# Kernel optimization log

Hardware: AMD Instinct MI355X
Metric: run time of the kernel (lower is better)

## Reference

```python
import jax, jax.numpy as jnp
import numpy as np

TOP_K = 8


def setup_inputs() -> dict:
    key = jax.random.key(0)
    ks = jax.random.split(key, 5)
    B, S, H, E, I = 2, 1024, 2048, 64, 768
    return {
        "hidden_states": jax.random.normal(ks[0], (B, S, H), dtype=jnp.float32),
        "router_w": jax.random.normal(ks[1], (H, E), dtype=jnp.float32) * 0.02,
        "gate_w": jax.random.normal(ks[2], (E, H, I), dtype=jnp.float32) * 0.02,
        "up_w": jax.random.normal(ks[3], (E, H, I), dtype=jnp.float32) * 0.02,
        "down_w": jax.random.normal(ks[4], (E, I, H), dtype=jnp.float32) * 0.02,
    }


def reference(hidden_states, router_w, gate_w, up_w, down_w):
    B, S, H = hidden_states.shape
    E = router_w.shape[1]
    x = hidden_states.reshape(-1, H)                      # [T, H]
    T = x.shape[0]

    router_logits = x @ router_w                           # [T, E]
    probs = jax.nn.softmax(router_logits.astype(jnp.float32), axis=-1)
    topk_w, topk_idx = jax.lax.top_k(probs, TOP_K)         # [T, K]
    topk_w = topk_w / jnp.sum(topk_w, axis=-1, keepdims=True)  # norm_topk_prob
    topk_w = topk_w.astype(x.dtype)

    # Dense combine weights: zero for non-selected experts -> same math as the
    # gather/scatter loop, jit-friendly (no data-dependent shapes).
    combine = jnp.zeros((T, E), dtype=x.dtype)
    combine = combine.at[jnp.arange(T)[:, None], topk_idx].set(topk_w)  # [T, E]

    g = jnp.einsum('th,ehi->tei', x, gate_w)               # [T, E, I]
    u = jnp.einsum('th,ehi->tei', x, up_w)                 # [T, E, I]
    h = jax.nn.silu(g) * u                                 # SwiGLU
    out = jnp.einsum('te,tei,eih->th', combine, h, down_w)  # weighted combine

    return out.reshape(B, S, H), router_logits
```

## Files before the change

kernel.cpp:

```cpp
#include <hip/hip_runtime.h>
#include <hip/hip_bf16.h>

typedef __hip_bfloat16 bf16;
typedef short s16x8 __attribute__((ext_vector_type(8)));
typedef unsigned short u16x8 __attribute__((ext_vector_type(8)));
typedef float f32x4 __attribute__((ext_vector_type(4)));

#define T_TOK 2048
#define HDIM  2048
#define NEXP  64
#define IDIM  768
#define TOPK  8
#define OUT_OFF (T_TOK * HDIM)
#define NPAIR (T_TOK * TOPK)

#define WS_TOPK_IDX  0
#define WS_TOPK_W    (64 * 1024)
#define WS_PAIR_TOK  (128 * 1024)
#define WS_SLOT_OF   (192 * 1024)
#define WS_COUNTS    (256 * 1024)
#define WS_OFFSETS   (257 * 1024)
#define WS_CURSOR    (258 * 1024)
#define WS_H         (1024 * 1024)
#define WS_PARTIAL   (WS_H + (size_t)NPAIR * IDIM * 2)
#define WS_XB        WS_PARTIAL

__device__ __forceinline__ float bf_to_f(unsigned short u) {
    return __uint_as_float(((unsigned int)u) << 16);
}
__device__ __forceinline__ unsigned short f2bf(float f) {
    unsigned int u = __float_as_uint(f);
    unsigned int r = (u + 0x7FFFu + ((u >> 16) & 1u)) >> 16;
    return (unsigned short)r;
}
__device__ __forceinline__ unsigned cvtpk(float lo, float hi) {
    unsigned r;
    asm("v_cvt_pk_bf16_f32 %0, %1, %2" : "=v"(r) : "v"(lo), "v"(hi));
    return r;
}

typedef const __attribute__((address_space(1))) unsigned int* gas_ptr;
typedef __attribute__((address_space(3))) unsigned int* las_ptr;
__device__ __forceinline__ void gload_lds16(const void* g, void* l) {
    __builtin_amdgcn_global_load_lds((gas_ptr)g, (las_ptr)l, 16, 0, 0);
}

__global__ __launch_bounds__(256) void xbf_kernel(const float* __restrict__ x,
                                                  unsigned short* __restrict__ xb) {
    int i = blockIdx.x * 256 + threadIdx.x;
    const float4* src = (const float4*)x + (size_t)i * 2;
    float4 a = src[0], b = src[1];
    u16x8 o;
    o[0] = f2bf(a.x); o[1] = f2bf(a.y); o[2] = f2bf(a.z); o[3] = f2bf(a.w);
    o[4] = f2bf(b.x); o[5] = f2bf(b.y); o[6] = f2bf(b.z); o[7] = f2bf(b.w);
    ((u16x8*)xb)[i] = o;
}

__global__ __launch_bounds__(256) void router_kernel(
    const float* __restrict__ x, const float* __restrict__ rw,
    float* __restrict__ logits) {
    int wave = threadIdx.x >> 6;
    int lane = threadIdx.x & 63;
    int t = blockIdx.x * 4 + wave;
    const float4* x4 = (const float4*)(x + (size_t)t * HDIM);
    float acc = 0.f;
    for (int h4 = 0; h4 < HDIM / 4; ++h4) {
        float4 xv = x4[h4];
        int h = h4 * 4;
        acc = fmaf(xv.x, rw[(h + 0) * NEXP + lane], acc);
        acc = fmaf(xv.y, rw[(h + 1) * NEXP + lane], acc);
        acc = fmaf(xv.z, rw[(h + 2) * NEXP + lane], acc);
        acc = fmaf(xv.w, rw[(h + 3) * NEXP + lane], acc);
    }
    logits[t * NEXP + lane] = acc;
}

__global__ __launch_bounds__(64) void topk_kernel(
    const float* __restrict__ logits, int* __restrict__ topk_idx,
    float* __restrict__ topk_w, int* __restrict__ counts) {
    int t = blockIdx.x;
    int lane = threadIdx.x;
    float lg = logits[t * NEXP + lane];
    float mx = lg;
    for (int off = 32; off; off >>= 1) mx = fmaxf(mx, __shfl_xor(mx, off));
    float ex = expf(lg - mx);
    float sum = ex;
    for (int off = 32; off; off >>= 1) sum += __shfl_xor(sum, off);
    float prob = ex / sum;

    float pr = prob;
    float myv = 0.f;
    int myidx = 0;
    float ksum = 0.f;
    for (int k = 0; k < TOPK; ++k) {
        float v = pr;
        int idx = lane;
        for (int off = 32; off; off >>= 1) {
            float ov = __shfl_xor(v, off);
            int oi = __shfl_xor(idx, off);
            if (ov > v || (ov == v && oi < idx)) { v = ov; idx = oi; }
        }
        ksum += v;
        if (lane == k) { myidx = idx; myv = v; }
        if (lane == idx) pr = -1.f;
    }
    if (lane < TOPK) {
        topk_idx[t * TOPK + lane] = myidx;
        topk_w[t * TOPK + lane] = myv / ksum;
        atomicAdd(&counts[myidx], 1);
    }
}

__global__ __launch_bounds__(64) void scan_kernel(
    const int* __restrict__ counts, int* __restrict__ offsets, int* __restrict__ cursor) {
    int lane = threadIdx.x;
    int c = counts[lane];
    int incl = c;
    for (int off = 1; off < 64; off <<= 1) {
        int tt = __shfl_up(incl, off);
        if (lane >= off) incl += tt;
    }
    offsets[lane] = incl - c;
    if (lane == 63) offsets[64] = incl;
    cursor[lane] = 0;
}

__global__ __launch_bounds__(256) void scatter_kernel(
    const int* __restrict__ topk_idx, const int* __restrict__ offsets,
    int* __restrict__ cursor, int* __restrict__ pair_token, int* __restrict__ slot_of) {
    int i = blockIdx.x * 256 + threadIdx.x;
    if (i >= NPAIR) return;
    int t = i >> 3;
    int e = topk_idx[i];
    int pos = atomicAdd(&cursor[e], 1);
    int slot = offsets[e] + pos;
    pair_token[slot] = t;
    slot_of[i] = slot;
}

#define BM   128
#define BKS  64

__global__ __launch_bounds__(512, 4) void gateup_mfma(
    const unsigned short* __restrict__ xb, const float* __restrict__ gate_w,
    const float* __restrict__ up_w, const int* __restrict__ offsets,
    const int* __restrict__ pair_token, unsigned short* __restrict__ hbuf) {
    int e = blockIdx.x;
    int ntile = blockIdx.z;
    int off = offsets[e];
    int cnt = offsets[e + 1] - off;
    if (cnt <= 0) return;

    __shared__ unsigned short As[2][BM * BKS];
    __shared__ unsigned short Bgu[2][BM * BKS];
    __shared__ int toks[BM];

    int tid = threadIdx.x;
    int lane = tid & 63;
    int wave = tid >> 6;
    int wr = wave >> 2, wc = wave & 3;
    int l15 = lane & 15, lg4 = lane >> 4;

    int mat = tid >> 8;
    int t8 = tid & 255;
    int nI2 = t8 & 31, kC = t8 >> 5;
    int brow0 = mat * 64 + nI2 * 2;
    int bslot = (kC ^ (nI2 & 7)) * 8;
    const float* bsrc = (mat ? up_w : gate_w) + (size_t)e * HDIM * IDIM
                        + (size_t)(kC * 8) * IDIM + ntile * 64 + nI2 * 2;

    for (int mt = blockIdx.y; mt * BM < cnt; mt += gridDim.y) {
        int m0 = mt * BM;
        if (tid < BM) {
            int p = m0 + tid;
            toks[tid] = pair_token[off + (p < cnt ? p : 0)];
        }
        __syncthreads();
        const unsigned short* aq[2];
        #pragma unroll
        for (int q = 0; q < 2; ++q) {
            int row = q * 64 + (tid >> 3);
            aq[q] = xb + (size_t)toks[row] * HDIM + (((tid & 7) ^ (row & 7)) * 8);
        }
        f32x4 accg[4] = {};
        f32x4 accu[4] = {};

        #pragma unroll
        for (int q = 0; q < 2; ++q)
            gload_lds16(aq[q], &As[0][(q * 512 + tid) * 8]);
        float2 Bv[8];
        #pragma unroll
        for (int i = 0; i < 8; ++i)
            Bv[i] = *(const float2*)(bsrc + (size_t)i * IDIM);

        for (int ks = 0; ks < HDIM / BKS; ++ks) {
            int p = ks & 1;
            {
                uint4 w0, w1;
                w0.x = cvtpk(Bv[0].x, Bv[1].x); w0.y = cvtpk(Bv[2].x, Bv[3].x);
                w0.z = cvtpk(Bv[4].x, Bv[5].x); w0.w = cvtpk(Bv[6].x, Bv[7].x);
                w1.x = cvtpk(Bv[0].y, Bv[1].y); w1.y = cvtpk(Bv[2].y, Bv[3].y);
                w1.z = cvtpk(Bv[4].y, Bv[5].y); w1.w = cvtpk(Bv[6].y, Bv[7].y);
                *(uint4*)&Bgu[p][brow0 * BKS + bslot] = w0;
                *(uint4*)&Bgu[p][(brow0 + 1) * BKS + bslot] = w1;
            }
            __syncthreads();
            if (ks + 1 < HDIM / BKS) {
                int h1 = (ks + 1) * BKS;
                #pragma unroll
                for (int q = 0; q < 2; ++q)
                    gload_lds16(aq[q] + h1, &As[p ^ 1][(q * 512 + tid) * 8]);
                #pragma unroll
                for (int i = 0; i < 8; ++i)
                    Bv[i] = *(const float2*)(bsrc + (size_t)(h1 + i) * IDIM);
            }
            #pragma unroll
            for (int kk = 0; kk < 2; ++kk) {
                int jk = kk * 4 + lg4;
                s16x8 a[4], bg, bu;
                #pragma unroll
                for (int mr = 0; mr < 4; ++mr) {
                    int r = wr * 64 + mr * 16 + l15;
                    a[mr] = *(const s16x8*)&As[p][r * BKS + ((jk ^ (r & 7)) * 8)];
                }
                int rg = wc * 16 + l15;
                int ru = 64 + rg;
                bg = *(const s16x8*)&Bgu[p][rg * BKS + ((jk ^ ((rg >> 1) & 7)) * 8)];
                bu = *(const s16x8*)&Bgu[p][ru * BKS + ((jk ^ ((ru >> 1) & 7)) * 8)];
                #pragma unroll
                for (int mr = 0; mr < 4; ++mr) {
                    accg[mr] = __builtin_amdgcn_mfma_f32_16x16x32_bf16(a[mr], bg, accg[mr], 0, 0, 0);
                    accu[mr] = __builtin_amdgcn_mfma_f32_16x16x32_bf16(a[mr], bu, accu[mr], 0, 0, 0);
                }
            }
        }

        int col = ntile * 64 + wc * 16 + l15;
        #pragma unroll
        for (int mr = 0; mr < 4; ++mr) {
            #pragma unroll
            for (int reg = 0; reg < 4; ++reg) {
                int r = m0 + wr * 64 + mr * 16 + lg4 * 4 + reg;
                if (r < cnt) {
                    float g = accg[mr][reg];
                    float u = accu[mr][reg];
                    float hv = (g / (1.f + __expf(-g))) * u;
                    hbuf[(size_t)(off + r) * IDIM + col] = f2bf(hv);
                }
            }
        }
        __syncthreads();
    }
}

__global__ __launch_bounds__(512, 4) void down_mfma(
    const unsigned short* __restrict__ hbuf, const float* __restrict__ down_w,
    const int* __restrict__ offsets, unsigned short* __restrict__ partial) {
    int e = blockIdx.x;
    int ntile = blockIdx.z;
    int off = offsets[e];
    int cnt = offsets[e + 1] - off;
    if (cnt <= 0) return;

    __shared__ unsigned short As[2][BM * BKS];
    __shared__ unsigned short Bd[2][BM * BKS];

    int tid = threadIdx.x;
    int lane = tid & 63;
    int wave = tid >> 6;
    int wr = wave >> 2, wc = wave & 3;
    int l15 = lane & 15, lg4 = lane >> 4;

    int nI2 = tid & 63, kC = tid >> 6;
    int brow0 = nI2 * 2;
    int bslot = (kC ^ (nI2 & 7)) * 8;
    const float* bsrc = down_w + (size_t)e * IDIM * HDIM
                        + (size_t)(kC * 8) * HDIM + ntile * 128 + nI2 * 2;

    for (int mt = blockIdx.y; mt * BM < cnt; mt += gridDim.y) {
        int m0 = mt * BM;
        const unsigned short* aq[2];
        #pragma unroll
        for (int q = 0; q < 2; ++q) {
            int row = q * 64 + (tid >> 3);
            int rr = m0 + row;
            if (rr >= cnt) rr = cnt - 1;
            aq[q] = hbuf + (size_t)(off + rr) * IDIM + (((tid & 7) ^ (row & 7)) * 8);
        }
        f32x4 acc[4][2] = {};

        #pragma unroll
        for (int q = 0; q < 2; ++q)
            gload_lds16(aq[q], &As[0][(q * 512 + tid) * 8]);
        float2 Bv[8];
        #pragma unroll
        for (int i = 0; i < 8; ++i)
            Bv[i] = *(const float2*)(bsrc + (size_t)i * HDIM);

        for (int ks = 0; ks < IDIM / BKS; ++ks) {
            int p = ks & 1;
            {
                uint4 w0, w1;
                w0.x = cvtpk(Bv[0].x, Bv[1].x); w0.y = cvtpk(Bv[2].x, Bv[3].x);
                w0.z = cvtpk(Bv[4].x, Bv[5].x); w0.w = cvtpk(Bv[6].x, Bv[7].x);
                w1.x = cvtpk(Bv[0].y, Bv[1].y); w1.y = cvtpk(Bv[2].y, Bv[3].y);
                w1.z = cvtpk(Bv[4].y, Bv[5].y); w1.w = cvtpk(Bv[6].y, Bv[7].y);
                *(uint4*)&Bd[p][brow0 * BKS + bslot] = w0;
                *(uint4*)&Bd[p][(brow0 + 1) * BKS + bslot] = w1;
            }
            __syncthreads();
            if (ks + 1 < IDIM / BKS) {
                int k1 = (ks + 1) * BKS;
                #pragma unroll
                for (int q = 0; q < 2; ++q)
                    gload_lds16(aq[q] + k1, &As[p ^ 1][(q * 512 + tid) * 8]);
                #pragma unroll
                for (int i = 0; i < 8; ++i)
                    Bv[i] = *(const float2*)(bsrc + (size_t)(k1 + i) * HDIM);
            }
            #pragma unroll
            for (int kk = 0; kk < 2; ++kk) {
                int jk = kk * 4 + lg4;
                s16x8 a[4], b[2];
                #pragma unroll
                for (int mr = 0; mr < 4; ++mr) {
                    int r = wr * 64 + mr * 16 + l15;
                    a[mr] = *(const s16x8*)&As[p][r * BKS + ((jk ^ (r & 7)) * 8)];
                }
                #pragma unroll
                for (int nr = 0; nr < 2; ++nr) {
                    int row = wc * 32 + nr * 16 + l15;
                    b[nr] = *(const s16x8*)&Bd[p][row * BKS + ((jk ^ ((row >> 1) & 7)) * 8)];
                }
                #pragma unroll
                for (int mr = 0; mr < 4; ++mr)
                    #pragma unroll
                    for (int nr = 0; nr < 2; ++nr)
                        acc[mr][nr] = __builtin_amdgcn_mfma_f32_16x16x32_bf16(
                            a[mr], b[nr], acc[mr][nr], 0, 0, 0);
            }
        }

        #pragma unroll
        for (int mr = 0; mr < 4; ++mr)
            #pragma unroll
            for (int nr = 0; nr < 2; ++nr) {
                int col = ntile * 128 + wc * 32 + nr * 16 + l15;
                #pragma unroll
                for (int reg = 0; reg < 4; ++reg) {
                    int r = m0 + wr * 64 + mr * 16 + lg4 * 4 + reg;
                    if (r < cnt)
                        partial[(size_t)(off + r) * HDIM + col] = f2bf(acc[mr][nr][reg]);
                }
            }
        __syncthreads();
    }
}

__global__ __launch_bounds__(256) void reduce_kernel(
    const unsigned short* __restrict__ partial, const int* __restrict__ slot_of,
    const float* __restrict__ topk_w, float* __restrict__ out) {
    int t = blockIdx.x;
    int j8 = threadIdx.x * 8;
    __shared__ int ss[8];
    __shared__ float sw[8];
    if (threadIdx.x < 8) {
        ss[threadIdx.x] = slot_of[t * TOPK + threadIdx.x];
        sw[threadIdx.x] = topk_w[t * TOPK + threadIdx.x];
    }
    __syncthreads();
    float acc[8] = {};
    #pragma unroll
    for (int k = 0; k < TOPK; ++k) {
        u16x8 v = *(const u16x8*)&partial[(size_t)ss[k] * HDIM + j8];
        float w = sw[k];
        #pragma unroll
        for (int i = 0; i < 8; ++i)
            acc[i] = fmaf(w, bf_to_f((unsigned short)v[i]), acc[i]);
    }
    float4 o0 = {acc[0], acc[1], acc[2], acc[3]};
    float4 o1 = {acc[4], acc[5], acc[6], acc[7]};
    *(float4*)&out[(size_t)t * HDIM + j8] = o0;
    *(float4*)&out[(size_t)t * HDIM + j8 + 4] = o1;
}

extern "C" void kernel_launch(void* const* d_in, const int* in_sizes, int n_in,
                              void* d_out, int out_size, void* d_ws, size_t ws_size,
                              hipStream_t stream) {
    const float* x  = (const float*)d_in[0];
    const float* rw = (const float*)d_in[1];
    const float* gw = (const float*)d_in[2];
    const float* uw = (const float*)d_in[3];
    const float* dw = (const float*)d_in[4];
    float* out = (float*)d_out;
    float* logits = out + OUT_OFF;

    char* ws = (char*)d_ws;
    int*   topk_idx   = (int*)(ws + WS_TOPK_IDX);
    float* topk_w     = (float*)(ws + WS_TOPK_W);
    int*   pair_token = (int*)(ws + WS_PAIR_TOK);
    int*   slot_of    = (int*)(ws + WS_SLOT_OF);
    int*   counts     = (int*)(ws + WS_COUNTS);
    int*   offsets    = (int*)(ws + WS_OFFSETS);
    int*   cursor     = (int*)(ws + WS_CURSOR);
    unsigned short* hbuf    = (unsigned short*)(ws + WS_H);
    unsigned short* partial = (unsigned short*)(ws + WS_PARTIAL);
    unsigned short* xb      = (unsigned short*)(ws + WS_XB);

    hipMemsetAsync(counts, 0, NEXP * sizeof(int), stream);
    xbf_kernel<<<T_TOK * HDIM / (256 * 8), 256, 0, stream>>>(x, xb);
    router_kernel<<<T_TOK / 4, 256, 0, stream>>>(x, rw, logits);
    topk_kernel<<<T_TOK, 64, 0, stream>>>(logits, topk_idx, topk_w, counts);
    scan_kernel<<<1, 64, 0, stream>>>(counts, offsets, cursor);
    scatter_kernel<<<NPAIR / 256, 256, 0, stream>>>(topk_idx, offsets, cursor, pair_token, slot_of);
    gateup_mfma<<<dim3(NEXP, 4, IDIM / 64), 512, 0, stream>>>(xb, gw, uw, offsets, pair_token, hbuf);
    down_mfma<<<dim3(NEXP, 4, HDIM / 128), 512, 0, stream>>>(hbuf, dw, offsets, partial);
    reduce_kernel<<<dim3(T_TOK, 1), 256, 0, stream>>>(partial, slot_of, topk_w, out);
}
```

Measured before the change: 674.1 us.

## Double-buffer weight registers and deepen prefetch with explicit waitcnt scheduling in MoE GEMMs

Both expert GEMM kernels now hold two register sets of fp32 weights, so weight loads are issued two K-steps ahead instead of one. The loop is unrolled by two and uses hand-placed s_waitcnt vmcnt(8) plus raw s_barrier and sched_barrier fences in place of __syncthreads. Each step then waits only for the older LDS-bound activation loads while the newer weight loads stay in flight. This is meant to hide more of the global-memory latency of streaming fp32 weights, at the cost of more VGPRs and fragile ordering assumptions about the memory counter.

```diff
diff --git a/kernel.cpp b/kernel.cpp
--- a/kernel.cpp
+++ b/kernel.cpp
@@ -140,6 +140,62 @@
 
 #define BM   128
 #define BKS  64
+#define NKG  (HDIM / BKS)
+#define NKD  (IDIM / BKS)
+
+#define GU_STEP(KS, BV, P)                                                    \
+  {                                                                           \
+            \
+    uint4 w0, w1;                                                             \
+    w0.x = cvtpk(BV[0].x, BV[1].x); w0.y = cvtpk(BV[2].x, BV[3].x);           \
+    w0.z = cvtpk(BV[4].x, BV[5].x); w0.w = cvtpk(BV[6].x, BV[7].x);           \
+    w1.x = cvtpk(BV[0].y, BV[1].y); w1.y = cvtpk(BV[2].y, BV[3].y);           \
+    w1.z = cvtpk(BV[4].y, BV[5].y); w1.w = cvtpk(BV[6].y, BV[7].y);           \
+    *(uint4*)&Bgu[P][brow0 * BKS + bslot] = w0;                               \
+    *(uint4*)&Bgu[P][(brow0 + 1) * BKS + bslot] = w1;                         \
+    __builtin_amdgcn_sched_barrier(0);                                        \
+    if ((KS) + 1 < NKG) {                                                     \
+      asm volatile("s_waitcnt vmcnt(8) lgkmcnt(0)" ::: "memory");             \
+    } else {                                                                  \
+      asm volatile("s_waitcnt vmcnt(0) lgkmcnt(0)" ::: "memory");             \
+    }                                                                         \
+    __builtin_amdgcn_s_barrier();                                             \
+    __builtin_amdgcn_sched_barrier(0);                                        \
+        \
+    if ((KS) + 1 < NKG) {                                                     \
+      int h1 = ((KS) + 1) * BKS;                                              \
+      gload_lds16(aq[0] + h1, &As[(P) ^ 1][(0 * 512 + tid) * 8]);             \
+      gload_lds16(aq[1] + h1, &As[(P) ^ 1][(1 * 512 + tid) * 8]);             \
+      __builtin_amdgcn_sched_barrier(0);                                      \
+    }                                                                         \
+    if ((KS) + 2 < NKG) {                                                     \
+      int h2 = ((KS) + 2) * BKS;                                              \
+      _Pragma("unroll")                                                       \
+      for (int i = 0; i < 8; ++i)                                             \
+        BV[i] = *(const float2*)(bsrc + (size_t)(h2 + i) * IDIM);             \
+      __builtin_amdgcn_sched_barrier(0);                                      \
+    }                                                                         \
+                                                    \
+    _Pragma("unroll")                                                         \
+    for (int kk = 0; kk < 2; ++kk) {                                          \
+      int jk = kk * 4 + lg4;                                                  \
+      s16x8 a[4], bg, bu;                                                     \
+      _Pragma("unroll")                                                       \
+      for (int mr = 0; mr < 4; ++mr) {                                        \
+        int r = wr * 64 + mr * 16 + l15;                                      \
+        a[mr] = *(const s16x8*)&As[P][r * BKS + ((jk ^ (r & 7)) * 8)];        \
+      }                                                                       \
+      int rg = wc * 16 + l15;                                                 \
+      int ru = 64 + rg;                                                       \
+      bg = *(const s16x8*)&Bgu[P][rg * BKS + ((jk ^ ((rg >> 1) & 7)) * 8)];   \
+      bu = *(const s16x8*)&Bgu[P][ru * BKS + ((jk ^ ((ru >> 1) & 7)) * 8)];   \
+      _Pragma("unroll")                                                       \
+      for (int mr = 0; mr < 4; ++mr) {                                        \
+        accg[mr] = __builtin_amdgcn_mfma_f32_16x16x32_bf16(a[mr], bg, accg[mr], 0, 0, 0); \
+        accu[mr] = __builtin_amdgcn_mfma_f32_16x16x32_bf16(a[mr], bu, accu[mr], 0, 0, 0); \
+      }                                                                       \
+    }                                                                         \
+  }
 
 __global__ __launch_bounds__(512, 4) void gateup_mfma(
     const unsigned short* __restrict__ xb, const float* __restrict__ gate_w,
@@ -157,8 +213,7 @@
 
     int tid = threadIdx.x;
     int lane = tid & 63;
-    int wave = tid >> 6;
-    int wr = wave >> 2, wc = wave & 3;
+    int wr = (tid >> 6) >> 2, wc = (tid >> 6) & 3;
     int l15 = lane & 15, lg4 = lane >> 4;
 
     int mat = tid >> 8;
@@ -185,54 +240,22 @@
         f32x4 accg[4] = {};
         f32x4 accu[4] = {};
 
-        #pragma unroll
-        for (int q = 0; q < 2; ++q)
-            gload_lds16(aq[q], &As[0][(q * 512 + tid) * 8]);
-        float2 Bv[8];
+        gload_lds16(aq[0], &As[0][(0 * 512 + tid) * 8]);
+        gload_lds16(aq[1], &As[0][(1 * 512 + tid) * 8]);
+        __builtin_amdgcn_sched_barrier(0);
+        float2 BvA[8], BvB[8];
         #pragma unroll
         for (int i = 0; i < 8; ++i)
-            Bv[i] = *(const float2*)(bsrc + (size_t)i * IDIM);
-
-        for (int ks = 0; ks < HDIM / BKS; ++ks) {
-            int p = ks & 1;
-            {
-                uint4 w0, w1;
-                w0.x = cvtpk(Bv[0].x, Bv[1].x); w0.y = cvtpk(Bv[2].x, Bv[3].x);
-                w0.z = cvtpk(Bv[4].x, Bv[5].x); w0.w = cvtpk(Bv[6].x, Bv[7].x);
-                w1.x = cvtpk(Bv[0].y, Bv[1].y); w1.y = cvtpk(Bv[2].y, Bv[3].y);
-                w1.z = cvtpk(Bv[4].y, Bv[5].y); w1.w = cvtpk(Bv[6].y, Bv[7].y);
-                *(uint4*)&Bgu[p][brow0 * BKS + bslot] = w0;
-                *(uint4*)&Bgu[p][(brow0 + 1) * BKS + bslot] = w1;
-            }
-            __syncthreads();
-            if (ks + 1 < HDIM / BKS) {
-                int h1 = (ks + 1) * BKS;
-                #pragma unroll
-                for (int q = 0; q < 2; ++q)
-                    gload_lds16(aq[q] + h1, &As[p ^ 1][(q * 512 + tid) * 8]);
-                #pragma unroll
-                for (int i = 0; i < 8; ++i)
-                    Bv[i] = *(const float2*)(bsrc + (size_t)(h1 + i) * IDIM);
-            }
-            #pragma unroll
-            for (int kk = 0; kk < 2; ++kk) {
-                int jk = kk * 4 + lg4;
-                s16x8 a[4], bg, bu;
-                #pragma unroll
-                for (int mr = 0; mr < 4; ++mr) {
-                    int r = wr * 64 + mr * 16 + l15;
-                    a[mr] = *(const s16x8*)&As[p][r * BKS + ((jk ^ (r & 7)) * 8)];
-                }
-                int rg = wc * 16 + l15;
-                int ru = 64 + rg;
-                bg = *(const s16x8*)&Bgu[p][rg * BKS + ((jk ^ ((rg >> 1) & 7)) * 8)];
-                bu = *(const s16x8*)&Bgu[p][ru * BKS + ((jk ^ ((ru >> 1) & 7)) * 8)];
-                #pragma unroll
-                for (int mr = 0; mr < 4; ++mr) {
-                    accg[mr] = __builtin_amdgcn_mfma_f32_16x16x32_bf16(a[mr], bg, accg[mr], 0, 0, 0);
-                    accu[mr] = __builtin_amdgcn_mfma_f32_16x16x32_bf16(a[mr], bu, accu[mr], 0, 0, 0);
-                }
-            }
+            BvA[i] = *(const float2*)(bsrc + (size_t)i * IDIM);
+        __builtin_amdgcn_sched_barrier(0);
+        #pragma unroll
+        for (int i = 0; i < 8; ++i)
+            BvB[i] = *(const float2*)(bsrc + (size_t)(BKS + i) * IDIM);
+        __builtin_amdgcn_sched_barrier(0);
+
+        for (int ks = 0; ks < NKG; ks += 2) {
+            GU_STEP(ks, BvA, 0);
+            GU_STEP(ks + 1, BvB, 1);
         }
 
         int col = ntile * 64 + wc * 16 + l15;
@@ -249,9 +272,60 @@
                 }
             }
         }
-        __syncthreads();
-    }
-}
+    }
+}
+
+#define DN_STEP(KS, BV, P)                                                    \
+  {                                                                           \
+    uint4 w0, w1;                                                             \
+    w0.x = cvtpk(BV[0].x, BV[1].x); w0.y = cvtpk(BV[2].x, BV[3].x);           \
+    w0.z = cvtpk(BV[4].x, BV[5].x); w0.w = cvtpk(BV[6].x, BV[7].x);           \
+    w1.x = cvtpk(BV[0].y, BV[1].y); w1.y = cvtpk(BV[2].y, BV[3].y);           \
+    w1.z = cvtpk(BV[4].y, BV[5].y); w1.w = cvtpk(BV[6].y, BV[7].y);           \
+    *(uint4*)&Bd[P][brow0 * BKS + bslot] = w0;                                \
+    *(uint4*)&Bd[P][(brow0 + 1) * BKS + bslot] = w1;                          \
+    __builtin_amdgcn_sched_barrier(0);                                        \
+    if ((KS) + 1 < NKD) {                                                     \
+      asm volatile("s_waitcnt vmcnt(8) lgkmcnt(0)" ::: "memory");             \
+    } else {                                                                  \
+      asm volatile("s_waitcnt vmcnt(0) lgkmcnt(0)" ::: "memory");             \
+    }                                                                         \
+    __builtin_amdgcn_s_barrier();                                             \
+    __builtin_amdgcn_sched_barrier(0);                                        \
+    if ((KS) + 1 < NKD) {                                                     \
+      int k1 = ((KS) + 1) * BKS;                                              \
+      gload_lds16(aq[0] + k1, &As[(P) ^ 1][(0 * 512 + tid) * 8]);             \
+      gload_lds16(aq[1] + k1, &As[(P) ^ 1][(1 * 512 + tid) * 8]);             \
+      __builtin_amdgcn_sched_barrier(0);                                      \
+    }                                                                         \
+    if ((KS) + 2 < NKD) {                                                     \
+      int k2 = ((KS) + 2) * BKS;                                              \
+      _Pragma("unroll")                                                       \
+      for (int i = 0; i < 8; ++i)                                             \
+        BV[i] = *(const float2*)(bsrc + (size_t)(k2 + i) * HDIM);             \
+      __builtin_amdgcn_sched_barrier(0);                                      \
+    }                                                                         \
+    _Pragma("unroll")                                                         \
+    for (int kk = 0; kk < 2; ++kk) {                                          \
+      int jk = kk * 4 + lg4;                                                  \
+      s16x8 a[4], b[2];                                                       \
+      _Pragma("unroll")                                                       \
+      for (int mr = 0; mr < 4; ++mr) {                                        \
+        int r = wr * 64 + mr * 16 + l15;                                      \
+        a[mr] = *(const s16x8*)&As[P][r * BKS + ((jk ^ (r & 7)) * 8)];        \
+      }                                                                       \
+      _Pragma("unroll")                                                       \
+      for (int nr = 0; nr < 2; ++nr) {                                        \
+        int row = wc * 32 + nr * 16 + l15;                                    \
+        b[nr] = *(const s16x8*)&Bd[P][row * BKS + ((jk ^ ((row >> 1) & 7)) * 8)]; \
+      }                                                                       \
+      _Pragma("unroll")                                                       \
+      for (int mr = 0; mr < 4; ++mr)                                          \
+        _Pragma("unroll")                                                     \
+        for (int nr = 0; nr < 2; ++nr)                                        \
+          acc[mr][nr] = __builtin_amdgcn_mfma_f32_16x16x32_bf16(a[mr], b[nr], acc[mr][nr], 0, 0, 0); \
+    }                                                                         \
+  }
 
 __global__ __launch_bounds__(512, 4) void down_mfma(
     const unsigned short* __restrict__ hbuf, const float* __restrict__ down_w,
@@ -267,8 +341,7 @@
 
     int tid = threadIdx.x;
     int lane = tid & 63;
-    int wave = tid >> 6;
-    int wr = wave >> 2, wc = wave & 3;
+    int wr = (tid >> 6) >> 2, wc = (tid >> 6) & 3;
     int l15 = lane & 15, lg4 = lane >> 4;
 
     int nI2 = tid & 63, kC = tid >> 6;
@@ -279,6 +352,7 @@
 
     for (int mt = blockIdx.y; mt * BM < cnt; mt += gridDim.y) {
         int m0 = mt * BM;
+        __syncthreads();
         const unsigned short* aq[2];
         #pragma unroll
         for (int q = 0; q < 2; ++q) {
@@ -289,56 +363,22 @@
         }
         f32x4 acc[4][2] = {};
 
-        #pragma unroll
-        for (int q = 0; q < 2; ++q)
-            gload_lds16(aq[q], &As[0][(q * 512 + tid) * 8]);
-        float2 Bv[8];
+        gload_lds16(aq[0], &As[0][(0 * 512 + tid) * 8]);
+        gload_lds16(aq[1], &As[0][(1 * 512 + tid) * 8]);
+        __builtin_amdgcn_sched_barrier(0);
+        float2 BvA[8], BvB[8];
         #pragma unroll
         for (int i = 0; i < 8; ++i)
-            Bv[i] = *(const float2*)(bsrc + (size_t)i * HDIM);
-
-        for (int ks = 0; ks < IDIM / BKS; ++ks) {
-            int p = ks & 1;
-            {
-                uint4 w0, w1;
-                w0.x = cvtpk(Bv[0].x, Bv[1].x); w0.y = cvtpk(Bv[2].x, Bv[3].x);
-                w0.z = cvtpk(Bv[4].x, Bv[5].x); w0.w = cvtpk(Bv[6].x, Bv[7].x);
-                w1.x = cvtpk(Bv[0].y, Bv[1].y); w1.y = cvtpk(Bv[2].y, Bv[3].y);
-                w1.z = cvtpk(Bv[4].y, Bv[5].y); w1.w = cvtpk(Bv[6].y, Bv[7].y);
-                *(uint4*)&Bd[p][brow0 * BKS + bslot] = w0;
-                *(uint4*)&Bd[p][(brow0 + 1) * BKS + bslot] = w1;
-            }
-            __syncthreads();
-            if (ks + 1 < IDIM / BKS) {
-                int k1 = (ks + 1) * BKS;
-                #pragma unroll
-                for (int q = 0; q < 2; ++q)
-                    gload_lds16(aq[q] + k1, &As[p ^ 1][(q * 512 + tid) * 8]);
-                #pragma unroll
-                for (int i = 0; i < 8; ++i)
-                    Bv[i] = *(const float2*)(bsrc + (size_t)(k1 + i) * HDIM);
-            }
-            #pragma unroll
-            for (int kk = 0; kk < 2; ++kk) {
-                int jk = kk * 4 + lg4;
-                s16x8 a[4], b[2];
-                #pragma unroll
-                for (int mr = 0; mr < 4; ++mr) {
-                    int r = wr * 64 + mr * 16 + l15;
-                    a[mr] = *(const s16x8*)&As[p][r * BKS + ((jk ^ (r & 7)) * 8)];
-                }
-                #pragma unroll
-                for (int nr = 0; nr < 2; ++nr) {
-                    int row = wc * 32 + nr * 16 + l15;
-                    b[nr] = *(const s16x8*)&Bd[p][row * BKS + ((jk ^ ((row >> 1) & 7)) * 8)];
-                }
-                #pragma unroll
-                for (int mr = 0; mr < 4; ++mr)
-                    #pragma unroll
-                    for (int nr = 0; nr < 2; ++nr)
-                        acc[mr][nr] = __builtin_amdgcn_mfma_f32_16x16x32_bf16(
-                            a[mr], b[nr], acc[mr][nr], 0, 0, 0);
-            }
+            BvA[i] = *(const float2*)(bsrc + (size_t)i * HDIM);
+        __builtin_amdgcn_sched_barrier(0);
+        #pragma unroll
+        for (int i = 0; i < 8; ++i)
+            BvB[i] = *(const float2*)(bsrc + (size_t)(BKS + i) * HDIM);
+        __builtin_amdgcn_sched_barrier(0);
+
+        for (int ks = 0; ks < NKD; ks += 2) {
+            DN_STEP(ks, BvA, 0);
+            DN_STEP(ks + 1, BvB, 1);
         }
 
         #pragma unroll
@@ -353,7 +393,6 @@
                         partial[(size_t)(off + r) * HDIM + col] = f2bf(acc[mr][nr][reg]);
                 }
             }
-        __syncthreads();
     }
 }
 
```

Result: slower. 736.8 us (+9.3%).

## Widen expert GEMM N-tiles, use 1024-thread blocks, and remap grid per XCD

Applied to the files above, without the earlier changes.

Both grouped expert GEMMs now run 1024-thread blocks that cover twice the output columns per tile: 128 for gate/up and 256 for down. Each gathered activation tile is therefore reused across more weight columns. The M-tile split per expert drops from 4 to 2, so each fp32 weight slice is streamed and converted fewer times. A flattened 1D grid puts all blocks of one expert on the same XCD, which should improve L2 sharing of the weight slices. The costs are a larger LDS footprint, which likely allows only one block per CU, and less parallelism for the load-imbalanced experts.

```diff
diff --git a/kernel.cpp b/kernel.cpp
--- a/kernel.cpp
+++ b/kernel.cpp
@@ -140,60 +140,63 @@
 
 #define BM   128
 #define BKS  64
-
-__global__ __launch_bounds__(512, 4) void gateup_mfma(
+#define NZG  6
+#define NZD  8
+#define NKG  (HDIM / BKS)
+#define NKD  (IDIM / BKS)
+
+__global__ __launch_bounds__(1024, 4) void gateup_mfma(
     const unsigned short* __restrict__ xb, const float* __restrict__ gate_w,
     const float* __restrict__ up_w, const int* __restrict__ offsets,
     const int* __restrict__ pair_token, unsigned short* __restrict__ hbuf) {
-    int e = blockIdx.x;
-    int ntile = blockIdx.z;
+    int id = blockIdx.x;
+    int xcd = id & 7, rid = id >> 3;
+    int ntile = rid % NZG;
+    int y = (rid / NZG) & 1;
+    int e = (rid / (2 * NZG)) * 8 + xcd;
     int off = offsets[e];
     int cnt = offsets[e + 1] - off;
     if (cnt <= 0) return;
 
     __shared__ unsigned short As[2][BM * BKS];
-    __shared__ unsigned short Bgu[2][BM * BKS];
+    __shared__ unsigned short Bgu[2][256 * BKS];
     __shared__ int toks[BM];
 
     int tid = threadIdx.x;
     int lane = tid & 63;
-    int wave = tid >> 6;
-    int wr = wave >> 2, wc = wave & 3;
+    int w = tid >> 6;
+    int wr = w & 1, wc = w >> 1;
     int l15 = lane & 15, lg4 = lane >> 4;
 
-    int mat = tid >> 8;
-    int t8 = tid & 255;
-    int nI2 = t8 & 31, kC = t8 >> 5;
-    int brow0 = mat * 64 + nI2 * 2;
+    int mat = tid >> 9;
+    int s = tid & 511;
+    int nI2 = s & 63, kC = s >> 6;
+    int brow0 = mat * 128 + nI2 * 2;
     int bslot = (kC ^ (nI2 & 7)) * 8;
     const float* bsrc = (mat ? up_w : gate_w) + (size_t)e * HDIM * IDIM
-                        + (size_t)(kC * 8) * IDIM + ntile * 64 + nI2 * 2;
-
-    for (int mt = blockIdx.y; mt * BM < cnt; mt += gridDim.y) {
+                        + (size_t)(kC * 8) * IDIM + ntile * 128 + nI2 * 2;
+
+    int arow = tid >> 3;
+    int ajx = (tid & 7) ^ (arow & 7);
+
+    for (int mt = y; mt * BM < cnt; mt += 2) {
         int m0 = mt * BM;
         if (tid < BM) {
             int p = m0 + tid;
             toks[tid] = pair_token[off + (p < cnt ? p : 0)];
         }
         __syncthreads();
-        const unsigned short* aq[2];
-        #pragma unroll
-        for (int q = 0; q < 2; ++q) {
-            int row = q * 64 + (tid >> 3);
-            aq[q] = xb + (size_t)toks[row] * HDIM + (((tid & 7) ^ (row & 7)) * 8);
-        }
+        const unsigned short* aq = xb + (size_t)toks[arow] * HDIM + ajx * 8;
         f32x4 accg[4] = {};
         f32x4 accu[4] = {};
 
-        #pragma unroll
-        for (int q = 0; q < 2; ++q)
-            gload_lds16(aq[q], &As[0][(q * 512 + tid) * 8]);
+        gload_lds16(aq, &As[0][tid * 8]);
         float2 Bv[8];
         #pragma unroll
         for (int i = 0; i < 8; ++i)
             Bv[i] = *(const float2*)(bsrc + (size_t)i * IDIM);
 
-        for (int ks = 0; ks < HDIM / BKS; ++ks) {
+        for (int ks = 0; ks < NKG; ++ks) {
             int p = ks & 1;
             {
                 uint4 w0, w1;
@@ -205,11 +208,9 @@
                 *(uint4*)&Bgu[p][(brow0 + 1) * BKS + bslot] = w1;
             }
             __syncthreads();
-            if (ks + 1 < HDIM / BKS) {
+            if (ks + 1 < NKG) {
                 int h1 = (ks + 1) * BKS;
-                #pragma unroll
-                for (int q = 0; q < 2; ++q)
-                    gload_lds16(aq[q] + h1, &As[p ^ 1][(q * 512 + tid) * 8]);
+                gload_lds16(aq + h1, &As[p ^ 1][tid * 8]);
                 #pragma unroll
                 for (int i = 0; i < 8; ++i)
                     Bv[i] = *(const float2*)(bsrc + (size_t)(h1 + i) * IDIM);
@@ -224,7 +225,7 @@
                     a[mr] = *(const s16x8*)&As[p][r * BKS + ((jk ^ (r & 7)) * 8)];
                 }
                 int rg = wc * 16 + l15;
-                int ru = 64 + rg;
+                int ru = 128 + rg;
                 bg = *(const s16x8*)&Bgu[p][rg * BKS + ((jk ^ ((rg >> 1) & 7)) * 8)];
                 bu = *(const s16x8*)&Bgu[p][ru * BKS + ((jk ^ ((ru >> 1) & 7)) * 8)];
                 #pragma unroll
@@ -235,7 +236,7 @@
             }
         }
 
-        int col = ntile * 64 + wc * 16 + l15;
+        int col = ntile * 128 + wc * 16 + l15;
         #pragma unroll
         for (int mr = 0; mr < 4; ++mr) {
             #pragma unroll
@@ -253,51 +254,51 @@
     }
 }
 
-__global__ __launch_bounds__(512, 4) void down_mfma(
+__global__ __launch_bounds__(1024, 4) void down_mfma(
     const unsigned short* __restrict__ hbuf, const float* __restrict__ down_w,
     const int* __restrict__ offsets, unsigned short* __restrict__ partial) {
-    int e = blockIdx.x;
-    int ntile = blockIdx.z;
+    int id = blockIdx.x;
+    int xcd = id & 7, rid = id >> 3;
+    int ntile = rid % NZD;
+    int y = (rid / NZD) & 1;
+    int e = (rid / (2 * NZD)) * 8 + xcd;
     int off = offsets[e];
     int cnt = offsets[e + 1] - off;
     if (cnt <= 0) return;
 
     __shared__ unsigned short As[2][BM * BKS];
-    __shared__ unsigned short Bd[2][BM * BKS];
+    __shared__ unsigned short Bd[2][256 * BKS];
 
     int tid = threadIdx.x;
     int lane = tid & 63;
-    int wave = tid >> 6;
-    int wr = wave >> 2, wc = wave & 3;
+    int w = tid >> 6;
+    int wr = w & 1, wc = w >> 1;
     int l15 = lane & 15, lg4 = lane >> 4;
 
-    int nI2 = tid & 63, kC = tid >> 6;
+    int nI2 = tid & 127, kC = tid >> 7;
     int brow0 = nI2 * 2;
     int bslot = (kC ^ (nI2 & 7)) * 8;
     const float* bsrc = down_w + (size_t)e * IDIM * HDIM
-                        + (size_t)(kC * 8) * HDIM + ntile * 128 + nI2 * 2;
-
-    for (int mt = blockIdx.y; mt * BM < cnt; mt += gridDim.y) {
+                        + (size_t)(kC * 8) * HDIM + ntile * 256 + nI2 * 2;
+
+    int arow = tid >> 3;
+    int ajx = (tid & 7) ^ (arow & 7);
+
+    for (int mt = y; mt * BM < cnt; mt += 2) {
         int m0 = mt * BM;
-        const unsigned short* aq[2];
-        #pragma unroll
-        for (int q = 0; q < 2; ++q) {
-            int row = q * 64 + (tid >> 3);
-            int rr = m0 + row;
-            if (rr >= cnt) rr = cnt - 1;
-            aq[q] = hbuf + (size_t)(off + rr) * IDIM + (((tid & 7) ^ (row & 7)) * 8);
-        }
+        __syncthreads();
+        int rr = m0 + arow;
+        if (rr >= cnt) rr = cnt - 1;
+        const unsigned short* aq = hbuf + (size_t)(off + rr) * IDIM + ajx * 8;
         f32x4 acc[4][2] = {};
 
-        #pragma unroll
-        for (int q = 0; q < 2; ++q)
-            gload_lds16(aq[q], &As[0][(q * 512 + tid) * 8]);
+        gload_lds16(aq, &As[0][tid * 8]);
         float2 Bv[8];
         #pragma unroll
         for (int i = 0; i < 8; ++i)
             Bv[i] = *(const float2*)(bsrc + (size_t)i * HDIM);
 
-        for (int ks = 0; ks < IDIM / BKS; ++ks) {
+        for (int ks = 0; ks < NKD; ++ks) {
             int p = ks & 1;
             {
                 uint4 w0, w1;
@@ -309,11 +310,9 @@
                 *(uint4*)&Bd[p][(brow0 + 1) * BKS + bslot] = w1;
             }
             __syncthreads();
-            if (ks + 1 < IDIM / BKS) {
+            if (ks + 1 < NKD) {
                 int k1 = (ks + 1) * BKS;
-                #pragma unroll
-                for (int q = 0; q < 2; ++q)
-                    gload_lds16(aq[q] + k1, &As[p ^ 1][(q * 512 + tid) * 8]);
+                gload_lds16(aq + k1, &As[p ^ 1][tid * 8]);
                 #pragma unroll
                 for (int i = 0; i < 8; ++i)
                     Bv[i] = *(const float2*)(bsrc + (size_t)(k1 + i) * HDIM);
@@ -345,7 +344,7 @@
         for (int mr = 0; mr < 4; ++mr)
             #pragma unroll
             for (int nr = 0; nr < 2; ++nr) {
-                int col = ntile * 128 + wc * 32 + nr * 16 + l15;
+                int col = ntile * 256 + wc * 32 + nr * 16 + l15;
                 #pragma unroll
                 for (int reg = 0; reg < 4; ++reg) {
                     int r = m0 + wr * 64 + mr * 16 + lg4 * 4 + reg;
@@ -413,7 +412,7 @@
     topk_kernel<<<T_TOK, 64, 0, stream>>>(logits, topk_idx, topk_w, counts);
     scan_kernel<<<1, 64, 0, stream>>>(counts, offsets, cursor);
     scatter_kernel<<<NPAIR / 256, 256, 0, stream>>>(topk_idx, offsets, cursor, pair_token, slot_of);
-    gateup_mfma<<<dim3(NEXP, 4, IDIM / 64), 512, 0, stream>>>(xb, gw, uw, offsets, pair_token, hbuf);
-    down_mfma<<<dim3(NEXP, 4, HDIM / 128), 512, 0, stream>>>(hbuf, dw, offsets, partial);
+    gateup_mfma<<<NEXP * 2 * NZG, 1024, 0, stream>>>(xb, gw, uw, offsets, pair_token, hbuf);
+    down_mfma<<<NEXP * 2 * NZD, 1024, 0, stream>>>(hbuf, dw, offsets, partial);
     reduce_kernel<<<dim3(T_TOK, 1), 256, 0, stream>>>(partial, slot_of, topk_w, out);
 }
```

After: 726.5 us. 1.08x slower.
